# Kernel optimization log

Measured on AMD Instinct MI355X. Metric: run time of the kernel, lower is better.

## Reference

```python
import jax, jax.numpy as jnp
import numpy as np

H, NH, HD = 1024, 16, 64
B, T, S = 2, 1024, 3
NOISE, STEP, TEMP, NSTEPS = 0.1, 0.01, 1.0, 5
LN_EPS = 1e-5


def setup_inputs() -> dict:
    key = jax.random.key(0)
    ks = jax.random.split(key, 9)
    return {
        "queries": jax.random.normal(ks[0], (B, NH, T, HD), jnp.float32),
        "keys": jax.random.normal(ks[1], (B, NH, T, HD), jnp.float32),
        "values": jax.random.normal(ks[2], (B, NH, T, HD), jnp.float32),
        "hidden_states": jax.random.normal(ks[3], (B, T, H), jnp.float32),
        "W1": jax.random.normal(ks[4], (H, H), jnp.float32) * 0.02,
        "b1": jnp.zeros((H,), jnp.float32),
        "ln_g": jnp.ones((H,), jnp.float32),
        "ln_b": jnp.zeros((H,), jnp.float32),
        "W2": jax.random.normal(ks[5], (H, H), jnp.float32) * 0.02,
        "b2": jnp.zeros((H,), jnp.float32),
        "hyp_noise": jax.random.normal(ks[6], (S, B, NH, T, HD), jnp.float32),
        "ref_noise": jax.random.normal(ks[7], (S, NSTEPS - 1, B, NH, T, HD), jnp.float32),
    }


def _attention_energy(q, k, v):
    # q: [S,B,H,T,D]; k,v: [B,H,T,D] -> energy [S,B]
    scores = jnp.einsum('sbhtd,bhud->sbhtu', q, k) / jnp.sqrt(jnp.float32(q.shape[-1]))
    attn = jax.nn.softmax(scores, axis=-1)
    out = jnp.einsum('sbhtu,bhud->sbhtd', attn, v)
    out_mag = jnp.linalg.norm(out, axis=-1).mean(axis=(2, 3))          # [S,B]
    entropy = -(attn * jnp.log(attn + 1e-8)).sum(axis=-1).mean(axis=(2, 3))
    align = (q * k[None]).sum(axis=-1).mean(axis=(2, 3))
    return out_mag - 0.1 * entropy - 0.05 * align


def reference(queries, keys, values, hidden_states, W1, b1, ln_g, ln_b, W2, b2,
              hyp_noise, ref_noise):
    # query_predictor: Linear -> LayerNorm -> ReLU -> Linear
    x = hidden_states @ W1.T + b1
    mu = x.mean(axis=-1, keepdims=True)
    var = ((x - mu) ** 2).mean(axis=-1, keepdims=True)
    x = (x - mu) / jnp.sqrt(var + LN_EPS) * ln_g + ln_b
    x = jax.nn.relu(x)
    ctx = x @ W2.T + b2                                   # [B,T,H]
    ctx = ctx.reshape(B, T, NH, HD).transpose(0, 2, 1, 3) # [B,NH,T,HD]

    # exploration hypotheses, refined jointly over the sample axis
    q = queries[None] + hyp_noise * NOISE                 # [S,B,NH,T,HD]
    for step in range(NSTEPS):
        q = q - STEP * (q - ctx[None])                    # PCN prediction-error update
        if step < NSTEPS - 1:
            q = q + ref_noise[:, step] * 0.01

    energies = _attention_energy(q, keys, values)         # [S,B]
    probs = jax.nn.softmax(-energies / TEMP, axis=0)      # [S,B]
    selected = jnp.einsum('sb,sbhtd->bhtd', probs, q)     # softmax-weighted mix
    return selected, keys, values
```

## Files before the change

kernel.cpp:

```cpp
#include <hip/hip_runtime.h>
#include <hip/hip_bf16.h>
#include <math.h>

#define NB 2
#define NHH 16
#define TT 1024
#define HDD 64
#define NSS 3
#define HH 1024

typedef float f4 __attribute__((ext_vector_type(4)));
typedef short bf16x8 __attribute__((ext_vector_type(8)));
typedef unsigned short u16;
typedef u16 u16x4 __attribute__((ext_vector_type(4)));

__device__ inline u16 f2bf(float f) {
    union { float f; unsigned u; } v; v.f = f;
    unsigned r = (v.u + 0x7FFFu + ((v.u >> 16) & 1u)) >> 16;
    return (u16)r;
}
__device__ inline float bf2f(u16 u) {
    union { unsigned u; float f; } v; v.u = ((unsigned)u) << 16;
    return v.f;
}
__device__ inline unsigned cvtpk(float lo, float hi) {
    unsigned r;
    asm("v_cvt_pk_bf16_f32 %0, %1, %2" : "=v"(r) : "v"(lo), "v"(hi));
    return r;
}
__device__ inline void gl_lds16(const u16* g, u16* l) {
    __builtin_amdgcn_global_load_lds(
        (const __attribute__((address_space(1))) unsigned int*)g,
        (__attribute__((address_space(3))) unsigned int*)l, 16, 0, 0);
}

__device__ inline float red16sum(float v) {
    v += __shfl_xor(v, 1);
    v += __shfl_xor(v, 2);
    v += __shfl_xor(v, 4);
    v += __shfl_xor(v, 8);
    return v;
}
__device__ inline float red64sum(float v) {
    v += __shfl_xor(v, 1);
    v += __shfl_xor(v, 2);
    v += __shfl_xor(v, 4);
    v += __shfl_xor(v, 8);
    v += __shfl_xor(v, 16);
    v += __shfl_xor(v, 32);
    return v;
}

__global__ __launch_bounds__(256) void k_prep(const float* __restrict__ hs, u16* __restrict__ hs_b,
                                              const float* __restrict__ W1, u16* __restrict__ w1_b,
                                              const float* __restrict__ W2, u16* __restrict__ w2_b,
                                              const float* __restrict__ keys, u16* __restrict__ k_b,
                                              float* __restrict__ outk,
                                              const float* __restrict__ V, u16* __restrict__ vt_b,
                                              float* __restrict__ outv) {
    __shared__ float tile[64][65];
    int b = blockIdx.x;
    if (b < 4096) {
        const float* s; u16* d; int base;
        if (b < 2048)      { s = hs; d = hs_b; base = 0; }
        else if (b < 3072) { s = W1; d = w1_b; base = 2048; }
        else               { s = W2; d = w2_b; base = 3072; }
        int i = (b - base) * 256 + threadIdx.x;
        f4 v = ((const f4*)s)[i];
        u16x4 o;
        o[0] = f2bf(v[0]); o[1] = f2bf(v[1]); o[2] = f2bf(v[2]); o[3] = f2bf(v[3]);
        ((u16x4*)d)[i] = o;
        return;
    }
    if (b < 5120) {
        int c = (b - 4096) * 256 + threadIdx.x;
        int bh = c >> 13, t = (c >> 3) & 1023, col8 = c & 7;
        int kt = t >> 6, row = t & 63;
        const float* sp = keys + (size_t)c * 8;
        f4 v0 = *(const f4*)(sp);
        f4 v1 = *(const f4*)(sp + 4);
        *(f4*)(outk + (size_t)c * 8) = v0;
        *(f4*)(outk + (size_t)c * 8 + 4) = v1;
        union { unsigned u[4]; int4 i4; } o;
        o.u[0] = cvtpk(v0[0] * 0.125f, v0[1] * 0.125f);
        o.u[1] = cvtpk(v0[2] * 0.125f, v0[3] * 0.125f);
        o.u[2] = cvtpk(v1[0] * 0.125f, v1[1] * 0.125f);
        o.u[3] = cvtpk(v1[2] * 0.125f, v1[3] * 0.125f);
        *(int4*)(k_b + (size_t)(bh * 16 + kt) * 4096 + row * 64 + ((col8 ^ (row & 7)) << 3)) = o.i4;
        return;
    }
    int idx = b - 5120;
    int bh = idx >> 4, kt = idx & 15, t0 = kt * 64;
    int r = threadIdx.x >> 2, c0 = (threadIdx.x & 3) * 16;
    const float* vp = V + ((size_t)bh * TT + t0) * HDD;
#pragma unroll
    for (int j = 0; j < 16; j += 4) {
        f4 v = *(const f4*)(vp + r * HDD + c0 + j);
        tile[r][c0 + j + 0] = v[0]; tile[r][c0 + j + 1] = v[1];
        tile[r][c0 + j + 2] = v[2]; tile[r][c0 + j + 3] = v[3];
        *(f4*)(outv + ((size_t)bh * TT + t0 + r) * HDD + c0 + j) = v;
    }
    __syncthreads();
    int d = threadIdx.x >> 2, x0 = (threadIdx.x & 3) * 16;
    u16* op = vt_b + (size_t)(bh * 16 + kt) * 4096 + d * 64;
#pragma unroll
    for (int cc = 0; cc < 2; ++cc) {
        int c8 = (x0 >> 3) + cc;
        union { unsigned u[4]; int4 i4; } o;
#pragma unroll
        for (int p = 0; p < 4; ++p)
            o.u[p] = cvtpk(tile[c8 * 8 + 2 * p][d], tile[c8 * 8 + 2 * p + 1][d]);
        *(int4*)(op + ((c8 ^ (d & 7)) << 3)) = o.i4;
    }
}

template <int EPI>
__global__ __launch_bounds__(256) void k_gemm_bt(const u16* __restrict__ A,
                                                 const u16* __restrict__ Bm,
                                                 const float* __restrict__ bias,
                                                 const float* __restrict__ que,
                                                 void* __restrict__ outv) {
    const int K = 1024, N = 1024;
    int w = threadIdx.x >> 6, l = threadIdx.x & 63, lr = l & 15, lg = l >> 4;
    int m0 = blockIdx.y * 64 + w * 16;
    int n0 = blockIdx.x * 64;
    const u16* ap = A + (size_t)(m0 + lr) * K + lg * 8;
    const u16* bp = Bm + (size_t)(n0 + lr) * K + lg * 8;
    f4 z4 = {0.f, 0.f, 0.f, 0.f};
    f4 acc[4] = {z4, z4, z4, z4};
#pragma unroll 2
    for (int kk = 0; kk < K; kk += 32) {
        bf16x8 a  = *(const bf16x8*)(ap + kk);
        bf16x8 b0 = *(const bf16x8*)(bp + kk);
        bf16x8 b1 = *(const bf16x8*)(bp + 16 * K + kk);
        bf16x8 b2 = *(const bf16x8*)(bp + 32 * K + kk);
        bf16x8 b3 = *(const bf16x8*)(bp + 48 * K + kk);
        acc[0] = __builtin_amdgcn_mfma_f32_16x16x32_bf16(a, b0, acc[0], 0, 0, 0);
        acc[1] = __builtin_amdgcn_mfma_f32_16x16x32_bf16(a, b1, acc[1], 0, 0, 0);
        acc[2] = __builtin_amdgcn_mfma_f32_16x16x32_bf16(a, b2, acc[2], 0, 0, 0);
        acc[3] = __builtin_amdgcn_mfma_f32_16x16x32_bf16(a, b3, acc[3], 0, 0, 0);
    }
    const float A5 = 0.9509900499f, CC = 1.0f - A5;
#pragma unroll
    for (int cf = 0; cf < 4; ++cf) {
        int col = n0 + cf * 16 + lr;
        float bs = bias[col];
#pragma unroll
        for (int r = 0; r < 4; ++r) {
            int row = m0 + lg * 4 + r;
            float v = acc[cf][r] + bs;
            if (EPI == 0) {
                ((u16*)outv)[(size_t)row * N + col] = f2bf(v);
            } else {
                int b = row >> 10, t = row & 1023, nh = col >> 6, hd = col & 63;
                size_t oidx = (((size_t)(b * NHH + nh)) * TT + t) * HDD + hd;
                ((float*)outv)[oidx] = A5 * que[oidx] + CC * v;
            }
        }
    }
}

__global__ __launch_bounds__(256) void k_lnrelu(const u16* __restrict__ X,
                                                const float* __restrict__ g,
                                                const float* __restrict__ bta,
                                                u16* __restrict__ xr) {
    int row = blockIdx.x;
    u16x4 xv = ((const u16x4*)(X + (size_t)row * HH))[threadIdx.x];
    f4 v;
    v[0] = bf2f(xv[0]); v[1] = bf2f(xv[1]); v[2] = bf2f(xv[2]); v[3] = bf2f(xv[3]);
    float s = v[0] + v[1] + v[2] + v[3];
    float s2 = v[0] * v[0] + v[1] * v[1] + v[2] * v[2] + v[3] * v[3];
    s = red64sum(s);
    s2 = red64sum(s2);
    __shared__ float red[8];
    int w = threadIdx.x >> 6, l = threadIdx.x & 63;
    if (l == 0) { red[w] = s; red[w + 4] = s2; }
    __syncthreads();
    float S1 = red[0] + red[1] + red[2] + red[3];
    float S2 = red[4] + red[5] + red[6] + red[7];
    float mu = S1 * (1.0f / 1024.0f);
    float var = S2 * (1.0f / 1024.0f) - mu * mu;
    float rstd = rsqrtf(var + 1e-5f);
    f4 gv = ((const f4*)g)[threadIdx.x];
    f4 bv = ((const f4*)bta)[threadIdx.x];
    u16x4 o;
#pragma unroll
    for (int j = 0; j < 4; ++j) {
        float y = (v[j] - mu) * rstd * gv[j] + bv[j];
        y = fmaxf(y, 0.f);
        o[j] = f2bf(y);
    }
    ((u16x4*)(xr + (size_t)row * HH))[threadIdx.x] = o;
}

__global__ __launch_bounds__(256, 3) void k_attn(const float* __restrict__ basep_,
                                                 const float* __restrict__ hyp,
                                                 const float* __restrict__ rn,
                                                 const u16* __restrict__ Kb,
                                                 const u16* __restrict__ Vt,
                                                 u16* __restrict__ qq,
                                                 float* __restrict__ part) {
    int bi = blockIdx.x;
    int p_ = bi & 31, j_ = bi >> 5;
    int h = p_ & 15, b = p_ >> 4;
    int s = j_ >> 3, qt2 = j_ & 7;
    int sb = s * 2 + b;
    int bh = b * NHH + h;
    int pi = sb * 128 + h * 8 + qt2;
    int w = threadIdx.x >> 6, l = threadIdx.x & 63, lr = l & 15, lg = l >> 4;
    int t0 = qt2 * 128;
    f4 z4 = {0.f, 0.f, 0.f, 0.f};

    __shared__ u16 Ks[2][4096];
    __shared__ u16 Vs[2][4096];
    __shared__ u16 plds[8][1024];

    const u16* kT = Kb + (size_t)(bh * 16) * 4096;
    const u16* vT = Vt + (size_t)(bh * 16) * 4096;

#pragma unroll
    for (int j = 0; j < 2; ++j) {
        int co = (w + 4 * j) * 512;
        gl_lds16(kT + co + l * 8, &Ks[0][co]);
        gl_lds16(vT + co + l * 8, &Vs[0][co]);
    }

    const float CH = 0.1f * 0.9509900499f;
    const float C0 = 0.0096059601f, C1 = 0.0097029900f, C2 = 0.0098010000f, C3 = 0.0099f;
    const float* basep = basep_ + (size_t)bh * TT * HDD;
    const float* hypp = hyp + ((size_t)(sb * NHH + h) * TT) * HDD;
    const float* rn0p = rn + ((size_t)(((s * 4 + 0) * 2 + b) * NHH + h) * TT) * HDD;
    const float* rn1p = rn + ((size_t)(((s * 4 + 1) * 2 + b) * NHH + h) * TT) * HDD;
    const float* rn2p = rn + ((size_t)(((s * 4 + 2) * 2 + b) * NHH + h) * TT) * HDD;
    const float* rn3p = rn + ((size_t)(((s * 4 + 3) * 2 + b) * NHH + h) * TT) * HDD;
    u16* qqp = qq + ((size_t)(sb * NHH + h) * TT) * HDD;

    char* slab = (char*)&plds[0][0];
    {
        int t = threadIdx.x;
#pragma unroll
        for (int m = 0; m < 4; ++m) {
            int j = t + 256 * m;
            size_t off = (size_t)t0 * HDD + (size_t)j * 8;
            f4 a0 = *(const f4*)(basep + off);
            f4 a1 = *(const f4*)(basep + off + 4);
            a0 += CH * __builtin_nontemporal_load((const f4*)(hypp + off));
            a1 += CH * __builtin_nontemporal_load((const f4*)(hypp + off + 4));
            a0 += C0 * __builtin_nontemporal_load((const f4*)(rn0p + off));
            a1 += C0 * __builtin_nontemporal_load((const f4*)(rn0p + off + 4));
            a0 += C1 * __builtin_nontemporal_load((const f4*)(rn1p + off));
            a1 += C1 * __builtin_nontemporal_load((const f4*)(rn1p + off + 4));
            a0 += C2 * __builtin_nontemporal_load((const f4*)(rn2p + off));
            a1 += C2 * __builtin_nontemporal_load((const f4*)(rn2p + off + 4));
            a0 += C3 * __builtin_nontemporal_load((const f4*)(rn3p + off));
            a1 += C3 * __builtin_nontemporal_load((const f4*)(rn3p + off + 4));
            union { unsigned u[4]; int4 i4; } o;
            o.u[0] = cvtpk(a0[0], a0[1]); o.u[1] = cvtpk(a0[2], a0[3]);
            o.u[2] = cvtpk(a1[0], a1[1]); o.u[3] = cvtpk(a1[2], a1[3]);
            int row = j >> 3, slot = j & 7;
            *(int4*)(slab + row * 128 + (((slot ^ (row & 7))) << 4)) = o.i4;
            *(int4*)(qqp + (size_t)t0 * HDD + (size_t)j * 8) = o.i4;
        }
    }
    __syncthreads();

    bf16x8 aq[2][2];
#pragma unroll
    for (int qr = 0; qr < 2; ++qr) {
        int r_ = w * 32 + qr * 16 + lr;
#pragma unroll
        for (int c = 0; c < 2; ++c)
            aq[qr][c] = *(const bf16x8*)(slab + r_ * 128 + (((c * 4 + lg) ^ (r_ & 7)) << 4));
    }

    f4 acco[2][4] = {{z4, z4, z4, z4}, {z4, z4, z4, z4}};
    float zrow[2][4] = {{0.f, 0.f, 0.f, 0.f}, {0.f, 0.f, 0.f, 0.f}};
    float wrow[2][4] = {{0.f, 0.f, 0.f, 0.f}, {0.f, 0.f, 0.f, 0.f}};
    float al_lane = 0.f;
    int kdiag = qt2 * 2 + (w >> 1);

    for (int kt = 0; kt < 16; ++kt) {
        int cur = kt & 1;
        if (kt < 15) {
#pragma unroll
            for (int j = 0; j < 2; ++j) {
                int co = (w + 4 * j) * 512;
                gl_lds16(kT + (kt + 1) * 4096 + co + l * 8, &Ks[cur ^ 1][co]);
                gl_lds16(vT + (kt + 1) * 4096 + co + l * 8, &Vs[cur ^ 1][co]);
            }
        }
        char* KsB = (char*)Ks[cur];
        char* VsB = (char*)Vs[cur];

        f4 sc[2][4];
        __builtin_amdgcn_s_setprio(1);
#pragma unroll
        for (int cf = 0; cf < 4; ++cf) {
            int row = cf * 16 + lr, rs = row & 7;
            bf16x8 bk0 = *(const bf16x8*)(KsB + row * 128 + ((lg ^ rs) << 4));
            bf16x8 bk1 = *(const bf16x8*)(KsB + row * 128 + (((4 + lg) ^ rs) << 4));
            f4 t0a = __builtin_amdgcn_mfma_f32_16x16x32_bf16(aq[0][0], bk0, z4, 0, 0, 0);
            sc[0][cf] = __builtin_amdgcn_mfma_f32_16x16x32_bf16(aq[0][1], bk1, t0a, 0, 0, 0);
            f4 t1a = __builtin_amdgcn_mfma_f32_16x16x32_bf16(aq[1][0], bk0, z4, 0, 0, 0);
            sc[1][cf] = __builtin_amdgcn_mfma_f32_16x16x32_bf16(aq[1][1], bk1, t1a, 0, 0, 0);
        }
        __builtin_amdgcn_s_setprio(0);

        if (kt == kdiag) {
            f4 sd0 = (w & 1) ? sc[0][2] : sc[0][0];
            f4 sd1 = (w & 1) ? sc[1][3] : sc[1][1];
            int rr = lr & 3;
            float e0 = rr == 0 ? sd0[0] : (rr == 1 ? sd0[1] : (rr == 2 ? sd0[2] : sd0[3]));
            float e1 = rr == 0 ? sd1[0] : (rr == 1 ? sd1[1] : (rr == 2 ? sd1[2] : sd1[3]));
            if (lg == (lr >> 2)) al_lane += (e0 + e1) * 8.0f;
        }

#pragma unroll
        for (int qr = 0; qr < 2; ++qr) {
            u16* pl = &plds[w * 2 + qr][0];
#pragma unroll
            for (int cf = 0; cf < 4; ++cf) {
                float p0 = __expf(sc[qr][cf][0]);
                float p1 = __expf(sc[qr][cf][1]);
                float p2 = __expf(sc[qr][cf][2]);
                float p3 = __expf(sc[qr][cf][3]);
                zrow[qr][0] += p0; zrow[qr][1] += p1;
                zrow[qr][2] += p2; zrow[qr][3] += p3;
                wrow[qr][0] = fmaf(p0, sc[qr][cf][0], wrow[qr][0]);
                wrow[qr][1] = fmaf(p1, sc[qr][cf][1], wrow[qr][1]);
                wrow[qr][2] = fmaf(p2, sc[qr][cf][2], wrow[qr][2]);
                wrow[qr][3] = fmaf(p3, sc[qr][cf][3], wrow[qr][3]);
                unsigned pa01 = cvtpk(p0, p1), pa23 = cvtpk(p2, p3);
                int base_ = cf * 16 + lr;
                pl[(((lg * 4 + 0) * 64 + base_)) ^ (((lg * 4 + 0) & 7) << 3)] = (u16)pa01;
                pl[(((lg * 4 + 1) * 64 + base_)) ^ (((lg * 4 + 1) & 7) << 3)] = (u16)(pa01 >> 16);
                pl[(((lg * 4 + 2) * 64 + base_)) ^ (((lg * 4 + 2) & 7) << 3)] = (u16)pa23;
                pl[(((lg * 4 + 3) * 64 + base_)) ^ (((lg * 4 + 3) & 7) << 3)] = (u16)(pa23 >> 16);
            }
        }
        bf16x8 pa[2][2];
#pragma unroll
        for (int qr = 0; qr < 2; ++qr) {
            const u16* pl = &plds[w * 2 + qr][0];
            pa[qr][0] = *(const bf16x8*)&pl[(lr * 64 + lg * 8) ^ ((lr & 7) << 3)];
            pa[qr][1] = *(const bf16x8*)&pl[(lr * 64 + 32 + lg * 8) ^ ((lr & 7) << 3)];
        }
        __builtin_amdgcn_s_setprio(1);
#pragma unroll
        for (int cf = 0; cf < 4; ++cf) {
            int row = cf * 16 + lr, rs = row & 7;
            bf16x8 bv0 = *(const bf16x8*)(VsB + row * 128 + ((lg ^ rs) << 4));
            bf16x8 bv1 = *(const bf16x8*)(VsB + row * 128 + (((4 + lg) ^ rs) << 4));
            acco[0][cf] = __builtin_amdgcn_mfma_f32_16x16x32_bf16(pa[0][0], bv0, acco[0][cf], 0, 0, 0);
            acco[0][cf] = __builtin_amdgcn_mfma_f32_16x16x32_bf16(pa[0][1], bv1, acco[0][cf], 0, 0, 0);
            acco[1][cf] = __builtin_amdgcn_mfma_f32_16x16x32_bf16(pa[1][0], bv0, acco[1][cf], 0, 0, 0);
            acco[1][cf] = __builtin_amdgcn_mfma_f32_16x16x32_bf16(pa[1][1], bv1, acco[1][cf], 0, 0, 0);
        }
        __builtin_amdgcn_s_setprio(0);

        __syncthreads();
    }

    float magw = 0.f, entw = 0.f;
#pragma unroll
    for (int qr = 0; qr < 2; ++qr) {
#pragma unroll
        for (int r = 0; r < 4; ++r) {
            float zz = red16sum(zrow[qr][r]);
            float ww = red16sum(wrow[qr][r]);
            float ssq = acco[qr][0][r] * acco[qr][0][r] + acco[qr][1][r] * acco[qr][1][r] +
                        acco[qr][2][r] * acco[qr][2][r] + acco[qr][3][r] * acco[qr][3][r];
            ssq = red16sum(ssq);
            float inv = 1.0f / zz;
            magw += sqrtf(ssq) * inv;
            entw += __logf(zz) - ww * inv;
        }
    }
    magw += __shfl_xor(magw, 16); magw += __shfl_xor(magw, 32);
    entw += __shfl_xor(entw, 16); entw += __shfl_xor(entw, 32);
    float al = red64sum(al_lane);

    __shared__ float red[4][3];
    if (l == 0) { red[w][0] = magw; red[w][1] = entw; red[w][2] = al; }
    __syncthreads();
    if (threadIdx.x == 0) {
        part[pi * 3 + 0] = red[0][0] + red[1][0] + red[2][0] + red[3][0];
        part[pi * 3 + 1] = red[0][1] + red[1][1] + red[2][1] + red[3][1];
        part[pi * 3 + 2] = red[0][2] + red[1][2] + red[2][2] + red[3][2];
    }
}

__global__ void k_finalize(const float* __restrict__ part, float* __restrict__ probs) {
    int w = threadIdx.x >> 6, l = threadIdx.x & 63;
    __shared__ float eng[6];
    if (w < 6) {
        float a0 = 0.f, a1 = 0.f, a2 = 0.f;
        for (int i = l; i < 128; i += 64) {
            const float* pp = part + (size_t)(w * 128 + i) * 3;
            a0 += pp[0]; a1 += pp[1]; a2 += pp[2];
        }
        a0 = red64sum(a0); a1 = red64sum(a1); a2 = red64sum(a2);
        if (l == 0) {
            const float inv = 1.0f / 16384.0f;
            eng[w] = a0 * inv - 0.1f * (a1 * inv) - 0.05f * (a2 * inv);
        }
    }
    __syncthreads();
    if (threadIdx.x < 2) {
        int b = threadIdx.x;
        float e0 = -eng[0 + b], e1 = -eng[2 + b], e2 = -eng[4 + b];
        float mx = fmaxf(e0, fmaxf(e1, e2));
        float x0 = __expf(e0 - mx), x1 = __expf(e1 - mx), x2 = __expf(e2 - mx);
        float inv = 1.0f / (x0 + x1 + x2);
        probs[0 + b] = x0 * inv;
        probs[2 + b] = x1 * inv;
        probs[4 + b] = x2 * inv;
    }
}

__global__ __launch_bounds__(256) void k_select(const u16* __restrict__ qq,
                                                const float* __restrict__ probs,
                                                float* __restrict__ out) {
    const int NQ4 = 524288;
    int i = blockIdx.x * 256 + threadIdx.x;
    int b = i >> 18;
    float p0 = probs[0 + b], p1 = probs[2 + b], p2 = probs[4 + b];
    u16x4 a0 = ((const u16x4*)qq)[i];
    u16x4 a1 = ((const u16x4*)qq)[NQ4 + i];
    u16x4 a2 = ((const u16x4*)qq)[2 * NQ4 + i];
    f4 v;
#pragma unroll
    for (int j = 0; j < 4; ++j)
        v[j] = p0 * bf2f(a0[j]) + p1 * bf2f(a1[j]) + p2 * bf2f(a2[j]);
    ((f4*)out)[i] = v;
}

extern "C" void kernel_launch(void* const* d_in, const int* in_sizes, int n_in,
                              void* d_out, int out_size, void* d_ws, size_t ws_size,
                              hipStream_t stream) {
    const float* queries = (const float*)d_in[0];
    const float* keys    = (const float*)d_in[1];
    const float* values  = (const float*)d_in[2];
    const float* hs      = (const float*)d_in[3];
    const float* W1      = (const float*)d_in[4];
    const float* b1      = (const float*)d_in[5];
    const float* ln_g    = (const float*)d_in[6];
    const float* ln_b    = (const float*)d_in[7];
    const float* W2      = (const float*)d_in[8];
    const float* b2      = (const float*)d_in[9];
    const float* hyp     = (const float*)d_in[10];
    const float* rn      = (const float*)d_in[11];
    float* out = (float*)d_out;
    char* ws = (char*)d_ws;

    const size_t MB = 1024ull * 1024ull;
    u16*   qq16 = (u16*)(ws);
    u16*   hs_b = (u16*)(ws + 0 * MB);
    u16*   w1_b = (u16*)(ws + 4 * MB);
    u16*   w2_b = (u16*)(ws + 6 * MB);
    u16*   X    = (u16*)(ws + 8 * MB);
    u16*   xr   = (u16*)(ws + 16 * MB);
    float* base = (float*)(ws + 24 * MB);
    u16*   k_b  = (u16*)(ws + 32 * MB);
    u16*   vt_b = (u16*)(ws + 36 * MB);
    float* part = (float*)(ws + 40 * MB);
    float* probs= (float*)(ws + 40 * MB + 65536);

    k_prep<<<5632, 256, 0, stream>>>(hs, hs_b, W1, w1_b, W2, w2_b,
                                     keys, k_b, out + 2097152,
                                     values, vt_b, out + 4194304);

    k_gemm_bt<0><<<dim3(16, 32), 256, 0, stream>>>(hs_b, w1_b, b1, nullptr, X);
    k_lnrelu<<<2048, 256, 0, stream>>>(X, ln_g, ln_b, xr);
    k_gemm_bt<1><<<dim3(16, 32), 256, 0, stream>>>(xr, w2_b, b2, queries, base);

    k_attn<<<768, 256, 0, stream>>>(base, hyp, rn, k_b, vt_b, qq16, part);
    k_finalize<<<1, 384, 0, stream>>>(part, probs);
    k_select<<<2048, 256, 0, stream>>>(qq16, probs, out);
}
```

Measured before the change: 168.0 us.

## Shrink attention LDS footprint to raise occupancy to four blocks per CU

The attention kernel's shared memory drops from 48KB to 32KB. K is now single-buffered and reloaded after a mid-iteration barrier, the Q staging slab reuses the second V buffer, and the P scratch is one buffer per wave, reused across the two query row groups. Launch bounds go from 3 to 4 blocks per CU to allow more resident waves for latency hiding. In exchange, each iteration gains an extra barrier, the K prefetch now waits until the QK step is done so it is exposed, and the PV matmuls are serialized per row group. Register pressure also tightens under the new launch bound.

```diff
diff --git a/kernel.cpp b/kernel.cpp
--- a/kernel.cpp
+++ b/kernel.cpp
@@ -193,7 +193,7 @@
     ((u16x4*)(xr + (size_t)row * HH))[threadIdx.x] = o;
 }
 
-__global__ __launch_bounds__(256, 3) void k_attn(const float* __restrict__ basep_,
+__global__ __launch_bounds__(256, 4) void k_attn(const float* __restrict__ basep_,
                                                  const float* __restrict__ hyp,
                                                  const float* __restrict__ rn,
                                                  const u16* __restrict__ Kb,
@@ -211,9 +211,11 @@
     int t0 = qt2 * 128;
     f4 z4 = {0.f, 0.f, 0.f, 0.f};
 
-    __shared__ u16 Ks[2][4096];
-    __shared__ u16 Vs[2][4096];
-    __shared__ u16 plds[8][1024];
+    __shared__ u16 LDSA[16384];
+    u16* Ks  = LDSA;
+    u16* Vs0 = LDSA + 4096;
+    u16* Vs1 = LDSA + 8192;
+    u16* plb = LDSA + 12288;
 
     const u16* kT = Kb + (size_t)(bh * 16) * 4096;
     const u16* vT = Vt + (size_t)(bh * 16) * 4096;
@@ -221,8 +223,8 @@
 #pragma unroll
     for (int j = 0; j < 2; ++j) {
         int co = (w + 4 * j) * 512;
-        gl_lds16(kT + co + l * 8, &Ks[0][co]);
-        gl_lds16(vT + co + l * 8, &Vs[0][co]);
+        gl_lds16(kT + co + l * 8, Ks + co);
+        gl_lds16(vT + co + l * 8, Vs0 + co);
     }
 
     const float CH = 0.1f * 0.9509900499f;
@@ -235,7 +237,7 @@
     const float* rn3p = rn + ((size_t)(((s * 4 + 3) * 2 + b) * NHH + h) * TT) * HDD;
     u16* qqp = qq + ((size_t)(sb * NHH + h) * TT) * HDD;
 
-    char* slab = (char*)&plds[0][0];
+    char* slab = (char*)Vs1;
     {
         int t = threadIdx.x;
 #pragma unroll
@@ -272,6 +274,7 @@
         for (int c = 0; c < 2; ++c)
             aq[qr][c] = *(const bf16x8*)(slab + r_ * 128 + (((c * 4 + lg) ^ (r_ & 7)) << 4));
     }
+    __syncthreads();
 
     f4 acco[2][4] = {{z4, z4, z4, z4}, {z4, z4, z4, z4}};
     float zrow[2][4] = {{0.f, 0.f, 0.f, 0.f}, {0.f, 0.f, 0.f, 0.f}};
@@ -281,16 +284,16 @@
 
     for (int kt = 0; kt < 16; ++kt) {
         int cur = kt & 1;
+        char* VcurB = (char*)(cur ? Vs1 : Vs0);
         if (kt < 15) {
+            u16* Vn = cur ? Vs0 : Vs1;
 #pragma unroll
             for (int j = 0; j < 2; ++j) {
                 int co = (w + 4 * j) * 512;
-                gl_lds16(kT + (kt + 1) * 4096 + co + l * 8, &Ks[cur ^ 1][co]);
-                gl_lds16(vT + (kt + 1) * 4096 + co + l * 8, &Vs[cur ^ 1][co]);
+                gl_lds16(vT + (kt + 1) * 4096 + co + l * 8, Vn + co);
             }
         }
-        char* KsB = (char*)Ks[cur];
-        char* VsB = (char*)Vs[cur];
+        char* KsB = (char*)Ks;
 
         f4 sc[2][4];
         __builtin_amdgcn_s_setprio(1);
@@ -315,9 +318,18 @@
             if (lg == (lr >> 2)) al_lane += (e0 + e1) * 8.0f;
         }
 
+        __syncthreads();
+        if (kt < 15) {
+#pragma unroll
+            for (int j = 0; j < 2; ++j) {
+                int co = (w + 4 * j) * 512;
+                gl_lds16(kT + (kt + 1) * 4096 + co + l * 8, Ks + co);
+            }
+        }
+
+        u16* pl = plb + w * 1024;
 #pragma unroll
         for (int qr = 0; qr < 2; ++qr) {
-            u16* pl = &plds[w * 2 + qr][0];
 #pragma unroll
             for (int cf = 0; cf < 4; ++cf) {
                 float p0 = __expf(sc[qr][cf][0]);
@@ -337,26 +349,19 @@
                 pl[(((lg * 4 + 2) * 64 + base_)) ^ (((lg * 4 + 2) & 7) << 3)] = (u16)pa23;
                 pl[(((lg * 4 + 3) * 64 + base_)) ^ (((lg * 4 + 3) & 7) << 3)] = (u16)(pa23 >> 16);
             }
-        }
-        bf16x8 pa[2][2];
-#pragma unroll
-        for (int qr = 0; qr < 2; ++qr) {
-            const u16* pl = &plds[w * 2 + qr][0];
-            pa[qr][0] = *(const bf16x8*)&pl[(lr * 64 + lg * 8) ^ ((lr & 7) << 3)];
-            pa[qr][1] = *(const bf16x8*)&pl[(lr * 64 + 32 + lg * 8) ^ ((lr & 7) << 3)];
-        }
-        __builtin_amdgcn_s_setprio(1);
-#pragma unroll
-        for (int cf = 0; cf < 4; ++cf) {
-            int row = cf * 16 + lr, rs = row & 7;
-            bf16x8 bv0 = *(const bf16x8*)(VsB + row * 128 + ((lg ^ rs) << 4));
-            bf16x8 bv1 = *(const bf16x8*)(VsB + row * 128 + (((4 + lg) ^ rs) << 4));
-            acco[0][cf] = __builtin_amdgcn_mfma_f32_16x16x32_bf16(pa[0][0], bv0, acco[0][cf], 0, 0, 0);
-            acco[0][cf] = __builtin_amdgcn_mfma_f32_16x16x32_bf16(pa[0][1], bv1, acco[0][cf], 0, 0, 0);
-            acco[1][cf] = __builtin_amdgcn_mfma_f32_16x16x32_bf16(pa[1][0], bv0, acco[1][cf], 0, 0, 0);
-            acco[1][cf] = __builtin_amdgcn_mfma_f32_16x16x32_bf16(pa[1][1], bv1, acco[1][cf], 0, 0, 0);
-        }
-        __builtin_amdgcn_s_setprio(0);
+            bf16x8 pa0 = *(const bf16x8*)&pl[(lr * 64 + lg * 8) ^ ((lr & 7) << 3)];
+            bf16x8 pa1 = *(const bf16x8*)&pl[(lr * 64 + 32 + lg * 8) ^ ((lr & 7) << 3)];
+            __builtin_amdgcn_s_setprio(1);
+#pragma unroll
+            for (int cf = 0; cf < 4; ++cf) {
+                int row = cf * 16 + lr, rs = row & 7;
+                bf16x8 bv0 = *(const bf16x8*)(VcurB + row * 128 + ((lg ^ rs) << 4));
+                bf16x8 bv1 = *(const bf16x8*)(VcurB + row * 128 + (((4 + lg) ^ rs) << 4));
+                acco[qr][cf] = __builtin_amdgcn_mfma_f32_16x16x32_bf16(pa0, bv0, acco[qr][cf], 0, 0, 0);
+                acco[qr][cf] = __builtin_amdgcn_mfma_f32_16x16x32_bf16(pa1, bv1, acco[qr][cf], 0, 0, 0);
+            }
+            __builtin_amdgcn_s_setprio(0);
+        }
 
         __syncthreads();
     }
```

New measurement: 183.3 us. 9.1% more time.
